# Performance work log

Measured on AMD Instinct MI355X. Metric: run time of the kernel, lower is better.

## Reference

```python
import jax, jax.numpy as jnp
import numpy as np

D_MODEL = 256
N_HEADS = 4
WINDOW = 8
DECAY = 0.9
STEP_SIZE = 0.5


def _linear(x, w, b):
    # torch nn.Linear: y = x @ w.T + b, w: [out, in]
    return jnp.einsum('...i,oi->...o', x, w) + b


def _layernorm(x, scale, bias, eps=1e-5):
    mu = jnp.mean(x, axis=-1, keepdims=True)
    var = jnp.var(x, axis=-1, keepdims=True)
    return (x - mu) * jax.lax.rsqrt(var + eps) * scale + bias


def _ema(x, decay):
    # ema[t] = decay*ema[t-1] + (1-decay)*x[t], ema[-1]=0
    # (exactly the causal conv with weights (1-d)*d^i from the torch code)
    def step(c, xt):
        c = decay * c + (1.0 - decay) * xt
        return c, c
    _, ys = jax.lax.scan(step, jnp.zeros_like(x[:, 0]), jnp.swapaxes(x, 0, 1))
    return jnp.swapaxes(ys, 0, 1)


def setup_inputs() -> dict:
    key = jax.random.key(0)
    ks = iter(jax.random.split(key, 40))
    B, T, D = 8, 1024, D_MODEL
    s = 0.02
    inp = {
        'parallel_repr': jax.random.normal(next(ks), (B, T, D), jnp.float32),
        'sequential_state': jax.random.normal(next(ks), (B, D), jnp.float32),
        'trajectory_summary': jax.random.normal(next(ks), (B, D), jnp.float32),
        # MultiheadAttention params
        'in_proj_w': jax.random.normal(next(ks), (3 * D, D), jnp.float32) * s,
        'in_proj_b': jnp.zeros((3 * D,), jnp.float32),
        'out_proj_w': jax.random.normal(next(ks), (D, D), jnp.float32) * s,
        'out_proj_b': jnp.zeros((D,), jnp.float32),
        # depthwise causal conv (local history)
        'conv_w': jax.random.normal(next(ks), (D, 1, WINDOW), jnp.float32) * s,
        'conv_b': jnp.zeros((D,), jnp.float32),
        # parallel_to_sequential / sequential_to_parallel
        'p2s_w': jax.random.normal(next(ks), (D, D), jnp.float32) * s,
        'p2s_b': jnp.zeros((D,), jnp.float32),
        's2p_w': jax.random.normal(next(ks), (D, D), jnp.float32) * s,
        's2p_b': jnp.zeros((D,), jnp.float32),
        # transition MLP: 3D -> 2D -> D
        'trans_w1': jax.random.normal(next(ks), (2 * D, 3 * D), jnp.float32) * s,
        'trans_b1': jnp.zeros((2 * D,), jnp.float32),
        'trans_w2': jax.random.normal(next(ks), (D, 2 * D), jnp.float32) * s,
        'trans_b2': jnp.zeros((D,), jnp.float32),
        # FFN: D -> 4D -> D
        'ffn_w1': jax.random.normal(next(ks), (4 * D, D), jnp.float32) * s,
        'ffn_b1': jnp.zeros((4 * D,), jnp.float32),
        'ffn_w2': jax.random.normal(next(ks), (D, 4 * D), jnp.float32) * s,
        'ffn_b2': jnp.zeros((D,), jnp.float32),
        # LayerNorms
        'ln1_s': jnp.ones((D,), jnp.float32), 'ln1_b': jnp.zeros((D,), jnp.float32),
        'ln2_s': jnp.ones((D,), jnp.float32), 'ln2_b': jnp.zeros((D,), jnp.float32),
        'ln3_s': jnp.ones((D,), jnp.float32), 'ln3_b': jnp.zeros((D,), jnp.float32),
        'ln4_s': jnp.ones((D,), jnp.float32), 'ln4_b': jnp.zeros((D,), jnp.float32),
    }
    return inp


def _forward(parallel_repr, sequential_state,
             in_proj_w, in_proj_b, out_proj_w, out_proj_b,
             conv_w, conv_b, p2s_w, p2s_b, s2p_w, s2p_b,
             trans_w1, trans_b1, trans_w2, trans_b2,
             ffn_w1, ffn_b1, ffn_w2, ffn_b2,
             ln1_s, ln1_b, ln2_s, ln2_b, ln3_s, ln3_b, ln4_s, ln4_b):
    B, T, D = parallel_repr.shape
    H, hd = N_HEADS, D // N_HEADS

    # --- causal self-attention (nn.MultiheadAttention, batch_first) ---
    qkv = _linear(parallel_repr, in_proj_w, in_proj_b)
    q, k, v = jnp.split(qkv, 3, axis=-1)
    q = q.reshape(B, T, H, hd)
    k = k.reshape(B, T, H, hd)
    v = v.reshape(B, T, H, hd)
    scores = jnp.einsum('bqhd,bkhd->bhqk', q, k) / jnp.sqrt(jnp.asarray(hd, q.dtype))
    causal = jnp.triu(jnp.ones((T, T), bool), 1)
    scores = jnp.where(causal, jnp.finfo(scores.dtype).min, scores)
    attn = jax.nn.softmax(scores, axis=-1)
    attn_out = jnp.einsum('bhqk,bkhd->bqhd', attn, v).reshape(B, T, D)
    attn_out = _linear(attn_out, out_proj_w, out_proj_b)
    x = _layernorm(parallel_repr + attn_out, ln1_s, ln1_b)

    # --- depthwise causal conv (local history) ---
    xt = jnp.swapaxes(x, 1, 2)  # [B, D, T]
    xt_pad = jnp.pad(xt, ((0, 0), (0, 0), (WINDOW - 1, 0)))
    local = jax.lax.conv_general_dilated(
        xt_pad, conv_w, window_strides=(1,), padding='VALID',
        dimension_numbers=('NCH', 'OIH', 'NCH'), feature_group_count=D)
    local_history = jnp.swapaxes(local + conv_b[None, :, None], 1, 2)  # [B, T, D]

    # --- global EMA summary ---
    global_summary = _ema(x, DECAY)

    # --- transition deltas + cumsum state integration ---
    parallel_guidance = _linear(x, p2s_w, p2s_b)
    combined = jnp.concatenate([x + 0.3 * parallel_guidance, local_history, global_summary], axis=-1)
    h = jax.nn.gelu(_linear(combined, trans_w1, trans_b1), approximate=False)
    deltas = _linear(h, trans_w2, trans_b2)
    states = sequential_state[:, None, :] + jnp.cumsum(deltas, axis=1) * STEP_SIZE
    states = _layernorm(states, ln3_s, ln3_b)

    # --- FFN with sequential guidance ---
    seq_guidance = _linear(states, s2p_w, s2p_b)
    f = jax.nn.gelu(_linear(x + 0.3 * seq_guidance, ffn_w1, ffn_b1), approximate=False)
    ffn_out = _linear(f, ffn_w2, ffn_b2)
    x = _layernorm(x + ffn_out, ln2_s, ln2_b)

    final_sequential_state = _layernorm(states[:, -1, :], ln4_s, ln4_b)
    final_trajectory_summary = global_summary[:, -1, :]
    return x, final_sequential_state, final_trajectory_summary


def reference(parallel_repr, sequential_state, trajectory_summary,
              in_proj_w, in_proj_b, out_proj_w, out_proj_b,
              conv_w, conv_b, p2s_w, p2s_b, s2p_w, s2p_b,
              trans_w1, trans_b1, trans_w2, trans_b2,
              ffn_w1, ffn_b1, ffn_w2, ffn_b2,
              ln1_s, ln1_b, ln2_s, ln2_b, ln3_s, ln3_b, ln4_s, ln4_b):
    # trajectory_summary is accepted by the torch forward but never used.
    return _forward(parallel_repr, sequential_state,
                    in_proj_w, in_proj_b, out_proj_w, out_proj_b,
                    conv_w, conv_b, p2s_w, p2s_b, s2p_w, s2p_b,
                    trans_w1, trans_b1, trans_w2, trans_b2,
                    ffn_w1, ffn_b1, ffn_w2, ffn_b2,
                    ln1_s, ln1_b, ln2_s, ln2_b, ln3_s, ln3_b, ln4_s, ln4_b)
```

## Files before the change

kernel.cpp:

```cpp
#include <hip/hip_runtime.h>
#include <math.h>

typedef unsigned short u16;
typedef __attribute__((ext_vector_type(8))) short bf16x8;
typedef __attribute__((ext_vector_type(4))) float f32x4;

#define D_MODEL 256
#define T_SZ 1024
constexpr size_t S_ELT = (size_t)8192 * 256;
constexpr size_t MB = 1024 * 1024;

constexpr size_t OFF_QKV = 0;
constexpr size_t OFF_ATTN = 12 * MB;
constexpr size_t OFF_F = 0;
constexpr size_t OFF_X = 16 * MB;
constexpr size_t OFF_COMB = 24 * MB;
constexpr size_t OFF_FB = 36 * MB;
constexpr size_t OFF_H = 44 * MB;
constexpr size_t OFF_XBF = 48 * MB;
constexpr size_t OFF_WB = 52 * MB;
constexpr size_t OFF_SCR1 = 55 * MB;
constexpr size_t OFF_SCR2 = 55 * MB + 262144;

constexpr int WB_INPROJ = 0;
constexpr int WB_OUTPROJ = 196608;
constexpr int WB_P2S = 262144;
constexpr int WB_S2P = 327680;
constexpr int WB_T1 = 393216;
constexpr int WB_T2 = 786432;
constexpr int WB_F1 = 917504;
constexpr int WB_F2 = 1179648;
constexpr int WB_TOTAL = 1441792;
constexpr int PR_TOTAL = 2097152;

__device__ __forceinline__ u16 f2bf(float f) {
  unsigned int u = __float_as_uint(f);
  u += 0x7fff + ((u >> 16) & 1);
  return (u16)(u >> 16);
}
__device__ __forceinline__ float bf2f(u16 s) {
  return __uint_as_float(((unsigned int)s) << 16);
}

__device__ __forceinline__ void glds16(const u16* g, u16* l) {
  __builtin_amdgcn_global_load_lds(
      (const __attribute__((address_space(1))) void*)g,
      (__attribute__((address_space(3))) void*)l, 16, 0, 0);
}

__global__ __launch_bounds__(256)
void wconv_kernel(const float* w0, const float* w1, const float* w2,
                  const float* w3, const float* w4, const float* w5,
                  const float* w6, const float* w7, const float* pr,
                  u16* __restrict__ wb, u16* __restrict__ prb) {
  const int idx4 = (blockIdx.x * 256 + threadIdx.x) * 4;
  if (idx4 < WB_TOTAL) {
    const int offs[9] = {WB_INPROJ, WB_OUTPROJ, WB_P2S,  WB_S2P, WB_T1,
                         WB_T2,     WB_F1,      WB_F2,   WB_TOTAL};
    const float* srcs[8] = {w0, w1, w2, w3, w4, w5, w6, w7};
    int seg = 0;
    while (idx4 >= offs[seg + 1]) ++seg;
    float4 v = *(const float4*)(srcs[seg] + (idx4 - offs[seg]));
    unsigned int lo = (unsigned int)f2bf(v.x) | ((unsigned int)f2bf(v.y) << 16);
    unsigned int hi = (unsigned int)f2bf(v.z) | ((unsigned int)f2bf(v.w) << 16);
    *(uint2*)(wb + idx4) = make_uint2(lo, hi);
  } else {
    const int i4 = idx4 - WB_TOTAL;
    if (i4 < PR_TOTAL) {
      float4 v = *(const float4*)(pr + i4);
      unsigned int lo = (unsigned int)f2bf(v.x) | ((unsigned int)f2bf(v.y) << 16);
      unsigned int hi = (unsigned int)f2bf(v.z) | ((unsigned int)f2bf(v.w) << 16);
      *(uint2*)(prb + i4) = make_uint2(lo, hi);
    }
  }
}

enum { EPI_NONE = 0, EPI_GELU = 1, EPI_ADDSCALE = 2 };

template <int EPI, int BM, int BN, bool OUTBF, bool VSPLIT>
__global__ __launch_bounds__(256, 4)
void mgemm(const u16* __restrict__ A, int lda,
           const u16* __restrict__ Wb, int K, const float* __restrict__ bias,
           void* __restrict__ Cv, int ldc, int col_off,
           const float* __restrict__ addsrc, u16* __restrict__ vt) {
  __shared__ u16 As[BM * 64];
  __shared__ u16 Bs[BN * 64];
  const int tid = threadIdx.x;
  const int w = tid >> 6, lane = tid & 63;
  const int ln = lane & 15, quad = lane >> 4;
  const int m0 = blockIdx.x * BM;
  const int n0 = blockIdx.y * BN;
  constexpr int MT = (BM == 128) ? 2 : 1;
  const int wm = w * (MT * 16);
  constexpr int wn = 0;
  constexpr int APW = BM / 64;
  constexpr int BPW = BN / 64;

  f32x4 acc[MT][4] = {};

  const int grow = lane >> 2;
  const int gk8 = (lane & 3) * 8;

  for (int k0 = 0; k0 < K; k0 += 64) {
#pragma unroll
    for (int s = 0; s < 2; ++s) {
#pragma unroll
      for (int p = 0; p < APW; ++p) {
        const int g = w * APW + p;
        glds16(A + (size_t)(m0 + g * 16 + grow) * lda + k0 + s * 32 + gk8,
               As + s * BM * 32 + g * 512);
      }
#pragma unroll
      for (int p = 0; p < BPW; ++p) {
        const int g = w * BPW + p;
        glds16(Wb + (size_t)(n0 + g * 16 + grow) * K + k0 + s * 32 + gk8,
               Bs + s * BN * 32 + g * 512);
      }
    }
    __syncthreads();
#pragma unroll
    for (int s = 0; s < 2; ++s) {
      const u16* abase = As + s * BM * 32 + (wm >> 4) * 512 + ln * 32 + quad * 8;
      const u16* bbase = Bs + s * BN * 32 + ln * 32 + quad * 8;
      bf16x8 af[MT], bv[4];
#pragma unroll
      for (int i = 0; i < MT; ++i) af[i] = *(const bf16x8*)(abase + i * 512);
#pragma unroll
      for (int j = 0; j < 4; ++j) bv[j] = *(const bf16x8*)(bbase + j * 512);
#pragma unroll
      for (int i = 0; i < MT; ++i)
#pragma unroll
        for (int j = 0; j < 4; ++j)
          acc[i][j] = __builtin_amdgcn_mfma_f32_16x16x32_bf16(af[i], bv[j],
                                                              acc[i][j], 0, 0, 0);
    }
    __syncthreads();
  }

#pragma unroll
  for (int i = 0; i < MT; ++i)
#pragma unroll
    for (int j = 0; j < 4; ++j) {
      const int col = n0 + wn + j * 16 + ln;
      const float bsv = bias[col];
      const int row0 = m0 + wm + i * 16 + quad * 4;
      float vals[4];
#pragma unroll
      for (int r = 0; r < 4; ++r) {
        float v = acc[i][j][r] + bsv;
        if (EPI == EPI_GELU) v = 0.5f * v * (1.0f + erff(v * 0.70710678f));
        if (EPI == EPI_ADDSCALE)
          v = addsrc[(size_t)(row0 + r) * 256 + col] + 0.3f * v;
        vals[r] = v;
      }
      if (VSPLIT && col >= 512) {
        ushort4 pk;
        pk.x = f2bf(vals[0]); pk.y = f2bf(vals[1]);
        pk.z = f2bf(vals[2]); pk.w = f2bf(vals[3]);
        *(ushort4*)(vt + (size_t)((row0 >> 10) * 256 + (col - 512)) * T_SZ +
                    (row0 & 1023)) = pk;
      } else if (OUTBF) {
#pragma unroll
        for (int r = 0; r < 4; ++r)
          ((u16*)Cv)[(size_t)(row0 + r) * ldc + col_off + col] = f2bf(vals[r]);
      } else {
#pragma unroll
        for (int r = 0; r < 4; ++r)
          ((float*)Cv)[(size_t)(row0 + r) * ldc + col_off + col] = vals[r];
      }
    }
}

__global__ __launch_bounds__(256)
void attn_flash(const u16* __restrict__ qkv, const u16* __restrict__ vt,
                u16* __restrict__ outp) {
  __shared__ u16 Ps[4][16][72];
  const int tid = threadIdx.x;
  const int w = tid >> 6, lane = tid & 63;
  const int ln = lane & 15, quad = lane >> 4, kq8 = quad * 8;
  const int wu = blockIdx.x * 4 + w;
  const int bh = wu >> 6, s = wu & 63;
  const int qt = (s & 1) ? (63 - (s >> 1)) : (s >> 1);
  const int q0 = qt * 16;
  const int b = bh >> 2, h = bh & 3;
  const u16* base = qkv + (size_t)b * T_SZ * 768;
  const u16* vbase = vt + (size_t)bh * 64 * T_SZ;

  bf16x8 qf[2];
#pragma unroll
  for (int ks = 0; ks < 2; ++ks)
    qf[ks] = *(const bf16x8*)(base + (size_t)(q0 + ln) * 768 + h * 64 +
                              ks * 32 + kq8);
  const short ob = (short)0x3F80;
  const bf16x8 ones = {ob, ob, ob, ob, ob, ob, ob, ob};

  f32x4 O[4] = {};
  f32x4 l_acc = {};
  const int ntiles = (qt >> 2) + 1;
  for (int jt = 0; jt < ntiles; ++jt) {
    const int c0 = jt * 64;
    f32x4 sv[4] = {};
#pragma unroll
    for (int ks = 0; ks < 2; ++ks)
#pragma unroll
      for (int j = 0; j < 4; ++j) {
        bf16x8 kf = *(const bf16x8*)(base + (size_t)(c0 + j * 16 + ln) * 768 +
                                     256 + h * 64 + ks * 32 + kq8);
        sv[j] = __builtin_amdgcn_mfma_f32_16x16x32_bf16(qf[ks], kf, sv[j], 0, 0, 0);
      }
    const bool need_mask = (c0 + 63 > q0);
#pragma unroll
    for (int j = 0; j < 4; ++j)
#pragma unroll
      for (int r = 0; r < 4; ++r) {
        float p = __expf(sv[j][r] * 0.125f);
        if (need_mask && (c0 + j * 16 + ln > q0 + quad * 4 + r)) p = 0.f;
        Ps[w][quad * 4 + r][j * 16 + ln] = f2bf(p);
      }
#pragma unroll
    for (int ks = 0; ks < 2; ++ks) {
      bf16x8 pf = *(const bf16x8*)&Ps[w][ln][ks * 32 + kq8];
      l_acc = __builtin_amdgcn_mfma_f32_16x16x32_bf16(pf, ones, l_acc, 0, 0, 0);
#pragma unroll
      for (int j = 0; j < 4; ++j) {
        bf16x8 vf = *(const bf16x8*)(vbase + (size_t)(j * 16 + ln) * T_SZ +
                                     c0 + ks * 32 + kq8);
        O[j] = __builtin_amdgcn_mfma_f32_16x16x32_bf16(pf, vf, O[j], 0, 0, 0);
      }
    }
  }
  u16* op = outp + (size_t)b * T_SZ * 256;
#pragma unroll
  for (int r = 0; r < 4; ++r) {
    const float inv = 1.f / l_acc[r];
#pragma unroll
    for (int j = 0; j < 4; ++j)
      op[(size_t)(q0 + quad * 4 + r) * 256 + h * 64 + j * 16 + ln] =
          f2bf(O[j][r] * inv);
  }
}

__device__ __forceinline__ float block_reduce_sum(float v, float* tmp) {
#pragma unroll
  for (int o = 32; o > 0; o >>= 1) v += __shfl_down(v, o);
  const int lane = threadIdx.x & 63, wid = threadIdx.x >> 6;
  if (lane == 0) tmp[wid] = v;
  __syncthreads();
  v = tmp[0] + tmp[1] + tmp[2] + tmp[3];
  __syncthreads();
  return v;
}

__device__ __forceinline__ float ln_finish(float v, float s1, float s2,
                                           float g, float bb) {
  float mean = s1 * (1.f / 256.f);
  float var = s2 * (1.f / 256.f) - mean * mean;
  return (v - mean) * rsqrtf(var + 1e-5f) * g + bb;
}

__global__ __launch_bounds__(256)
void ln_add_kernel(const float* __restrict__ a, const float* __restrict__ addsrc,
                   const float* __restrict__ g, const float* __restrict__ bb,
                   float* __restrict__ outp, u16* __restrict__ obf) {
  __shared__ float tmp[4];
  const size_t row = blockIdx.x;
  const int d = threadIdx.x;
  float v = a[row * 256 + d] + addsrc[row * 256 + d];
  float s1 = block_reduce_sum(v, tmp);
  float s2 = block_reduce_sum(v * v, tmp);
  float y = ln_finish(v, s1, s2, g[d], bb[d]);
  outp[row * 256 + d] = y;
  if (obf) obf[row * 256 + d] = f2bf(y);
}

__global__ __launch_bounds__(256)
void ln3_states_kernel(const float* __restrict__ deltas, const float* __restrict__ scr,
                       const float* __restrict__ seq, const float* __restrict__ g,
                       const float* __restrict__ bb, u16* __restrict__ st) {
  __shared__ float tmp[4];
  const int row = blockIdx.x;
  const int b = row >> 10, t = row & 1023;
  const int d = threadIdx.x;
  float v = seq[b * 256 + d] +
            0.5f * (deltas[(size_t)row * 256 + d] +
                    scr[(size_t)(b * 32 + (t >> 5)) * 256 + d]);
  float s1 = block_reduce_sum(v, tmp);
  float s2 = block_reduce_sum(v * v, tmp);
  st[(size_t)row * 256 + d] = f2bf(ln_finish(v, s1, s2, g[d], bb[d]));
}

__global__ __launch_bounds__(256)
void ln4_kernel(const u16* __restrict__ st, const float* __restrict__ g,
                const float* __restrict__ bb, float* __restrict__ outp) {
  __shared__ float tmp[4];
  const int b = blockIdx.x, d = threadIdx.x;
  float v = bf2f(st[(size_t)(b * T_SZ + 1023) * 256 + d]);
  float s1 = block_reduce_sum(v, tmp);
  float s2 = block_reduce_sum(v * v, tmp);
  outp[b * 256 + d] = ln_finish(v, s1, s2, g[d], bb[d]);
}

__global__ __launch_bounds__(256)
void emaconv_kernel(const float* __restrict__ x, const float* __restrict__ cw,
                    const float* __restrict__ cb, u16* __restrict__ comb,
                    float* __restrict__ scr) {
  const int bc = blockIdx.x;
  const int b = bc >> 5, ch = bc & 31;
  const int d = threadIdx.x;
  const int t0 = ch * 32;
  float wreg[8];
#pragma unroll
  for (int j = 0; j < 8; ++j) wreg[j] = cw[d * 8 + j];
  const float bias = cb[d];
  float xw[8];
#pragma unroll
  for (int j = 0; j < 7; ++j) {
    const int ts = t0 - 7 + j;
    xw[j] = (ts >= 0) ? x[(size_t)(b * T_SZ + ts) * 256 + d] : 0.f;
  }
  float c = 0.f;
#pragma unroll
  for (int tl = 0; tl < 32; ++tl) {
    const size_t row = (size_t)(b * T_SZ + t0 + tl);
    xw[7] = x[row * 256 + d];
    float conv = bias;
#pragma unroll
    for (int j = 0; j < 8; ++j) conv = fmaf(xw[j], wreg[j], conv);
    c = 0.9f * c + 0.1f * xw[7];
    comb[row * 768 + 256 + d] = f2bf(conv);
    comb[row * 768 + 512 + d] = f2bf(c);
#pragma unroll
    for (int j = 0; j < 7; ++j) xw[j] = xw[j + 1];
  }
  scr[(size_t)bc * 256 + d] = c;
}

__global__ __launch_bounds__(256)
void ema_b_kernel(float* __restrict__ scr) {
  const int b = blockIdx.x, d = threadIdx.x;
  const float q32 = 0.03433683820292512f;
  float carry = 0.f;
  for (int ch = 0; ch < 32; ++ch) {
    const size_t idx = (size_t)(b * 32 + ch) * 256 + d;
    float e = scr[idx];
    scr[idx] = carry;
    carry = e + q32 * carry;
  }
}

__global__ __launch_bounds__(256)
void ema_c_kernel(u16* __restrict__ comb, const float* __restrict__ scr,
                  float* __restrict__ fts) {
  const int row = blockIdx.x;
  const int b = row >> 10, t = row & 1023;
  const int d = threadIdx.x;
  const int ch = t >> 5, tl = t & 31;
  float carry = scr[(size_t)(b * 32 + ch) * 256 + d];
  float l = bf2f(comb[(size_t)row * 768 + 512 + d]);
  float y = fmaf(__powf(0.9f, (float)(tl + 1)), carry, l);
  comb[(size_t)row * 768 + 512 + d] = f2bf(y);
  if (t == 1023) fts[b * 256 + d] = y;
}

__global__ __launch_bounds__(256)
void cs_a_kernel(float* __restrict__ deltas, float* __restrict__ scr) {
  const int bc = blockIdx.x;
  const int b = bc >> 5, ch = bc & 31;
  const int d = threadIdx.x;
  const int t0 = ch * 32;
  float c = 0.f;
  for (int tl = 0; tl < 32; ++tl) {
    const size_t idx = (size_t)(b * T_SZ + t0 + tl) * 256 + d;
    c += deltas[idx];
    deltas[idx] = c;
  }
  scr[(size_t)bc * 256 + d] = c;
}

__global__ __launch_bounds__(256)
void cs_b_kernel(float* __restrict__ scr) {
  const int b = blockIdx.x, d = threadIdx.x;
  float carry = 0.f;
  for (int ch = 0; ch < 32; ++ch) {
    const size_t idx = (size_t)(b * 32 + ch) * 256 + d;
    float e = scr[idx];
    scr[idx] = carry;
    carry += e;
  }
}

extern "C" void kernel_launch(void* const* d_in, const int* in_sizes, int n_in,
                              void* d_out, int out_size, void* d_ws,
                              size_t ws_size, hipStream_t stream) {
  (void)in_sizes; (void)n_in; (void)out_size; (void)ws_size;
  const float* parallel_repr = (const float*)d_in[0];
  const float* sequential_state = (const float*)d_in[1];
  const float* in_proj_b = (const float*)d_in[4];
  const float* out_proj_b = (const float*)d_in[6];
  const float* conv_w = (const float*)d_in[7];
  const float* conv_b = (const float*)d_in[8];
  const float* p2s_b = (const float*)d_in[10];
  const float* s2p_b = (const float*)d_in[12];
  const float* trans_b1 = (const float*)d_in[14];
  const float* trans_b2 = (const float*)d_in[16];
  const float* ffn_b1 = (const float*)d_in[18];
  const float* ffn_b2 = (const float*)d_in[20];
  const float* ln1_s = (const float*)d_in[21];
  const float* ln1_b = (const float*)d_in[22];
  const float* ln2_s = (const float*)d_in[23];
  const float* ln2_b = (const float*)d_in[24];
  const float* ln3_s = (const float*)d_in[25];
  const float* ln3_b = (const float*)d_in[26];
  const float* ln4_s = (const float*)d_in[27];
  const float* ln4_b = (const float*)d_in[28];

  char* ws = (char*)d_ws;
  u16* qkv_bf = (u16*)(ws + OFF_QKV);
  u16* attn_bf = (u16*)(ws + OFF_ATTN);
  u16* states_bf = (u16*)(ws + OFF_ATTN);
  u16* f_bf = (u16*)(ws + OFF_F);
  float* x = (float*)(ws + OFF_X);
  u16* comb = (u16*)(ws + OFF_COMB);
  u16* pr_bf = (u16*)(ws + OFF_COMB);
  u16* ffn_in = (u16*)(ws + OFF_COMB);
  float* fbuf = (float*)(ws + OFF_FB);
  u16* vt = (u16*)(ws + OFF_H);
  u16* h_bf = (u16*)(ws + OFF_H);
  u16* x_bf = (u16*)(ws + OFF_XBF);
  u16* wb = (u16*)(ws + OFF_WB);
  float* scr1 = (float*)(ws + OFF_SCR1);
  float* scr2 = (float*)(ws + OFF_SCR2);
  float* out = (float*)d_out;
  float* out_fss = out + S_ELT;
  float* out_fts = out + S_ELT + 2048;

  const dim3 blk(256);

  wconv_kernel<<<3456, blk, 0, stream>>>(
      (const float*)d_in[3], (const float*)d_in[5], (const float*)d_in[9],
      (const float*)d_in[11], (const float*)d_in[13], (const float*)d_in[15],
      (const float*)d_in[17], (const float*)d_in[19], parallel_repr, wb, pr_bf);
  mgemm<EPI_NONE, 128, 64, true, true><<<dim3(64, 12), blk, 0, stream>>>(
      pr_bf, 256, wb + WB_INPROJ, 256, in_proj_b, qkv_bf, 768, 0, nullptr, vt);
  attn_flash<<<512, blk, 0, stream>>>(qkv_bf, vt, attn_bf);
  mgemm<EPI_NONE, 64, 64, false, false><<<dim3(128, 4), blk, 0, stream>>>(
      attn_bf, 256, wb + WB_OUTPROJ, 256, out_proj_b, fbuf, 256, 0, nullptr,
      nullptr);
  ln_add_kernel<<<8192, blk, 0, stream>>>(parallel_repr, fbuf, ln1_s, ln1_b, x,
                                          x_bf);
  emaconv_kernel<<<256, blk, 0, stream>>>(x, conv_w, conv_b, comb, scr1);
  ema_b_kernel<<<8, blk, 0, stream>>>(scr1);
  ema_c_kernel<<<8192, blk, 0, stream>>>(comb, scr1, out_fts);
  mgemm<EPI_ADDSCALE, 64, 64, true, false><<<dim3(128, 4), blk, 0, stream>>>(
      x_bf, 256, wb + WB_P2S, 256, p2s_b, comb, 768, 0, x, nullptr);
  mgemm<EPI_GELU, 128, 64, true, false><<<dim3(64, 8), blk, 0, stream>>>(
      comb, 768, wb + WB_T1, 768, trans_b1, h_bf, 512, 0, nullptr, nullptr);
  mgemm<EPI_NONE, 64, 64, false, false><<<dim3(128, 4), blk, 0, stream>>>(
      h_bf, 512, wb + WB_T2, 512, trans_b2, fbuf, 256, 0, nullptr, nullptr);
  cs_a_kernel<<<256, blk, 0, stream>>>(fbuf, scr2);
  cs_b_kernel<<<8, blk, 0, stream>>>(scr2);
  ln3_states_kernel<<<8192, blk, 0, stream>>>(fbuf, scr2, sequential_state,
                                              ln3_s, ln3_b, states_bf);
  ln4_kernel<<<8, blk, 0, stream>>>(states_bf, ln4_s, ln4_b, out_fss);
  mgemm<EPI_ADDSCALE, 64, 64, true, false><<<dim3(128, 4), blk, 0, stream>>>(
      states_bf, 256, wb + WB_S2P, 256, s2p_b, ffn_in, 256, 0, x, nullptr);
  mgemm<EPI_GELU, 128, 64, true, false><<<dim3(64, 16), blk, 0, stream>>>(
      ffn_in, 256, wb + WB_F1, 256, ffn_b1, f_bf, 1024, 0, nullptr, nullptr);
  mgemm<EPI_NONE, 64, 64, false, false><<<dim3(128, 4), blk, 0, stream>>>(
      f_bf, 1024, wb + WB_F2, 1024, ffn_b2, fbuf, 256, 0, nullptr, nullptr);
  ln_add_kernel<<<8192, blk, 0, stream>>>(x, fbuf, ln2_s, ln2_b, out, nullptr);
}
```

Before: 275.9 us.

## Fuse LayerNorm into GEMM epilogues and merge scan stages via cooperative launches

Adds a full-row GEMM kernel (64x256 tile) that applies bias, residual add and LayerNorm in its epilogue, replacing the out-proj and FFN2 GEMMs plus their separate ln_add kernels. The three-kernel EMA scan and the cumsum+LN3+LN4 sequence each become a single cooperative kernel that uses grid.sync, keeping per-thread partials in registers instead of round-tripping through global memory. This removes several launches and full-tensor passes, but the fused GEMM runs only 128 blocks (lower occupancy), and the csln kernel performs 32 block reductions serially per block.

```diff
diff --git a/kernel.cpp b/kernel.cpp
--- a/kernel.cpp
+++ b/kernel.cpp
@@ -1,4 +1,5 @@
 #include <hip/hip_runtime.h>
+#include <hip/hip_cooperative_groups.h>
 #include <math.h>
 
 typedef unsigned short u16;
@@ -171,6 +172,92 @@
     }
 }
 
+template <bool WRITE_BF>
+__global__ __launch_bounds__(256, 2)
+void mgemm_ln(const u16* __restrict__ A, const u16* __restrict__ Wb, int K,
+              const float* __restrict__ bias, const float* __restrict__ addsrc,
+              const float* __restrict__ g, const float* __restrict__ bb,
+              float* __restrict__ outf, u16* __restrict__ outbf) {
+  __shared__ u16 As[64 * 64];
+  __shared__ u16 Bs[256 * 64];
+  const int tid = threadIdx.x;
+  const int w = tid >> 6, lane = tid & 63;
+  const int ln = lane & 15, quad = lane >> 4;
+  const int m0 = blockIdx.x * 64;
+  const int grow = lane >> 2;
+  const int gk8 = (lane & 3) * 8;
+
+  f32x4 acc[16] = {};
+
+  for (int k0 = 0; k0 < K; k0 += 64) {
+#pragma unroll
+    for (int s = 0; s < 2; ++s) {
+      glds16(A + (size_t)(m0 + w * 16 + grow) * K + k0 + s * 32 + gk8,
+             As + s * 2048 + w * 512);
+#pragma unroll
+      for (int p = 0; p < 4; ++p) {
+        const int gg = w * 4 + p;
+        glds16(Wb + (size_t)(gg * 16 + grow) * K + k0 + s * 32 + gk8,
+               Bs + s * 8192 + gg * 512);
+      }
+    }
+    __syncthreads();
+#pragma unroll
+    for (int s = 0; s < 2; ++s) {
+      const u16* abase = As + s * 2048 + w * 512 + ln * 32 + quad * 8;
+      const u16* bbase = Bs + s * 8192 + ln * 32 + quad * 8;
+      bf16x8 af = *(const bf16x8*)abase;
+#pragma unroll
+      for (int j = 0; j < 16; ++j) {
+        bf16x8 bv = *(const bf16x8*)(bbase + j * 512);
+        acc[j] = __builtin_amdgcn_mfma_f32_16x16x32_bf16(af, bv, acc[j], 0, 0, 0);
+      }
+    }
+    __syncthreads();
+  }
+
+  const int row0 = m0 + w * 16 + quad * 4;
+  float s1[4] = {}, s2[4] = {};
+#pragma unroll
+  for (int j = 0; j < 16; ++j) {
+    const int col = j * 16 + ln;
+    const float bsv = bias[col];
+#pragma unroll
+    for (int r = 0; r < 4; ++r) {
+      float v = acc[j][r] + bsv + addsrc[(size_t)(row0 + r) * 256 + col];
+      acc[j][r] = v;
+      s1[r] += v;
+      s2[r] += v * v;
+    }
+  }
+#pragma unroll
+  for (int r = 0; r < 4; ++r) {
+#pragma unroll
+    for (int o = 8; o > 0; o >>= 1) {
+      s1[r] += __shfl_xor(s1[r], o);
+      s2[r] += __shfl_xor(s2[r], o);
+    }
+  }
+  float mean[4], inv[4];
+#pragma unroll
+  for (int r = 0; r < 4; ++r) {
+    mean[r] = s1[r] * (1.f / 256.f);
+    float var = s2[r] * (1.f / 256.f) - mean[r] * mean[r];
+    inv[r] = rsqrtf(var + 1e-5f);
+  }
+#pragma unroll
+  for (int j = 0; j < 16; ++j) {
+    const int col = j * 16 + ln;
+    const float gc = g[col], bc = bb[col];
+#pragma unroll
+    for (int r = 0; r < 4; ++r) {
+      const float y = (acc[j][r] - mean[r]) * inv[r] * gc + bc;
+      outf[(size_t)(row0 + r) * 256 + col] = y;
+      if (WRITE_BF) outbf[(size_t)(row0 + r) * 256 + col] = f2bf(y);
+    }
+  }
+}
+
 __global__ __launch_bounds__(256)
 void attn_flash(const u16* __restrict__ qkv, const u16* __restrict__ vt,
                 u16* __restrict__ outp) {
@@ -240,15 +327,18 @@
   }
 }
 
-__device__ __forceinline__ float block_reduce_sum(float v, float* tmp) {
-#pragma unroll
-  for (int o = 32; o > 0; o >>= 1) v += __shfl_down(v, o);
+__device__ __forceinline__ void block_reduce_2(float& a, float& q, float* tmp) {
+#pragma unroll
+  for (int o = 32; o > 0; o >>= 1) {
+    a += __shfl_down(a, o);
+    q += __shfl_down(q, o);
+  }
   const int lane = threadIdx.x & 63, wid = threadIdx.x >> 6;
-  if (lane == 0) tmp[wid] = v;
+  if (lane == 0) { tmp[wid] = a; tmp[4 + wid] = q; }
   __syncthreads();
-  v = tmp[0] + tmp[1] + tmp[2] + tmp[3];
+  a = tmp[0] + tmp[1] + tmp[2] + tmp[3];
+  q = tmp[4] + tmp[5] + tmp[6] + tmp[7];
   __syncthreads();
-  return v;
 }
 
 __device__ __forceinline__ float ln_finish(float v, float s1, float s2,
@@ -259,51 +349,10 @@
 }
 
 __global__ __launch_bounds__(256)
-void ln_add_kernel(const float* __restrict__ a, const float* __restrict__ addsrc,
-                   const float* __restrict__ g, const float* __restrict__ bb,
-                   float* __restrict__ outp, u16* __restrict__ obf) {
-  __shared__ float tmp[4];
-  const size_t row = blockIdx.x;
-  const int d = threadIdx.x;
-  float v = a[row * 256 + d] + addsrc[row * 256 + d];
-  float s1 = block_reduce_sum(v, tmp);
-  float s2 = block_reduce_sum(v * v, tmp);
-  float y = ln_finish(v, s1, s2, g[d], bb[d]);
-  outp[row * 256 + d] = y;
-  if (obf) obf[row * 256 + d] = f2bf(y);
-}
-
-__global__ __launch_bounds__(256)
-void ln3_states_kernel(const float* __restrict__ deltas, const float* __restrict__ scr,
-                       const float* __restrict__ seq, const float* __restrict__ g,
-                       const float* __restrict__ bb, u16* __restrict__ st) {
-  __shared__ float tmp[4];
-  const int row = blockIdx.x;
-  const int b = row >> 10, t = row & 1023;
-  const int d = threadIdx.x;
-  float v = seq[b * 256 + d] +
-            0.5f * (deltas[(size_t)row * 256 + d] +
-                    scr[(size_t)(b * 32 + (t >> 5)) * 256 + d]);
-  float s1 = block_reduce_sum(v, tmp);
-  float s2 = block_reduce_sum(v * v, tmp);
-  st[(size_t)row * 256 + d] = f2bf(ln_finish(v, s1, s2, g[d], bb[d]));
-}
-
-__global__ __launch_bounds__(256)
-void ln4_kernel(const u16* __restrict__ st, const float* __restrict__ g,
-                const float* __restrict__ bb, float* __restrict__ outp) {
-  __shared__ float tmp[4];
-  const int b = blockIdx.x, d = threadIdx.x;
-  float v = bf2f(st[(size_t)(b * T_SZ + 1023) * 256 + d]);
-  float s1 = block_reduce_sum(v, tmp);
-  float s2 = block_reduce_sum(v * v, tmp);
-  outp[b * 256 + d] = ln_finish(v, s1, s2, g[d], bb[d]);
-}
-
-__global__ __launch_bounds__(256)
-void emaconv_kernel(const float* __restrict__ x, const float* __restrict__ cw,
-                    const float* __restrict__ cb, u16* __restrict__ comb,
-                    float* __restrict__ scr) {
+void emaconv_coop(const float* __restrict__ x, const float* __restrict__ cw,
+                  const float* __restrict__ cb, u16* __restrict__ comb,
+                  float* __restrict__ scr, float* __restrict__ fts) {
+  cooperative_groups::grid_group grid = cooperative_groups::this_grid();
   const int bc = blockIdx.x;
   const int b = bc >> 5, ch = bc & 31;
   const int d = threadIdx.x;
@@ -318,6 +367,7 @@
     const int ts = t0 - 7 + j;
     xw[j] = (ts >= 0) ? x[(size_t)(b * T_SZ + ts) * 256 + d] : 0.f;
   }
+  float lreg[32];
   float c = 0.f;
 #pragma unroll
   for (int tl = 0; tl < 32; ++tl) {
@@ -327,65 +377,85 @@
 #pragma unroll
     for (int j = 0; j < 8; ++j) conv = fmaf(xw[j], wreg[j], conv);
     c = 0.9f * c + 0.1f * xw[7];
+    lreg[tl] = c;
     comb[row * 768 + 256 + d] = f2bf(conv);
-    comb[row * 768 + 512 + d] = f2bf(c);
 #pragma unroll
     for (int j = 0; j < 7; ++j) xw[j] = xw[j + 1];
   }
   scr[(size_t)bc * 256 + d] = c;
+  grid.sync();
+  if (bc < 8) {
+    const float q32 = 0.03433683820292512f;
+    float carry = 0.f;
+    for (int chh = 0; chh < 32; ++chh) {
+      const size_t idx = (size_t)(bc * 32 + chh) * 256 + d;
+      float e = scr[idx];
+      scr[idx] = carry;
+      carry = e + q32 * carry;
+    }
+  }
+  grid.sync();
+  const float carry = scr[(size_t)bc * 256 + d];
+  float pw = 0.9f;
+  float ylast = 0.f;
+#pragma unroll
+  for (int tl = 0; tl < 32; ++tl) {
+    const size_t row = (size_t)(b * T_SZ + t0 + tl);
+    const float y = fmaf(pw, carry, lreg[tl]);
+    comb[row * 768 + 512 + d] = f2bf(y);
+    pw *= 0.9f;
+    ylast = y;
+  }
+  if (ch == 31) fts[b * 256 + d] = ylast;
 }
 
 __global__ __launch_bounds__(256)
-void ema_b_kernel(float* __restrict__ scr) {
-  const int b = blockIdx.x, d = threadIdx.x;
-  const float q32 = 0.03433683820292512f;
-  float carry = 0.f;
-  for (int ch = 0; ch < 32; ++ch) {
-    const size_t idx = (size_t)(b * 32 + ch) * 256 + d;
-    float e = scr[idx];
-    scr[idx] = carry;
-    carry = e + q32 * carry;
-  }
-}
-
-__global__ __launch_bounds__(256)
-void ema_c_kernel(u16* __restrict__ comb, const float* __restrict__ scr,
-                  float* __restrict__ fts) {
-  const int row = blockIdx.x;
-  const int b = row >> 10, t = row & 1023;
-  const int d = threadIdx.x;
-  const int ch = t >> 5, tl = t & 31;
-  float carry = scr[(size_t)(b * 32 + ch) * 256 + d];
-  float l = bf2f(comb[(size_t)row * 768 + 512 + d]);
-  float y = fmaf(__powf(0.9f, (float)(tl + 1)), carry, l);
-  comb[(size_t)row * 768 + 512 + d] = f2bf(y);
-  if (t == 1023) fts[b * 256 + d] = y;
-}
-
-__global__ __launch_bounds__(256)
-void cs_a_kernel(float* __restrict__ deltas, float* __restrict__ scr) {
+void csln_coop(const float* __restrict__ deltas, const float* __restrict__ seq,
+               const float* __restrict__ g3, const float* __restrict__ b3,
+               const float* __restrict__ g4, const float* __restrict__ b4,
+               float* __restrict__ scr, u16* __restrict__ st,
+               float* __restrict__ fss) {
+  cooperative_groups::grid_group grid = cooperative_groups::this_grid();
+  __shared__ float tmp[8];
   const int bc = blockIdx.x;
   const int b = bc >> 5, ch = bc & 31;
   const int d = threadIdx.x;
   const int t0 = ch * 32;
+  float cum[32];
   float c = 0.f;
+#pragma unroll
   for (int tl = 0; tl < 32; ++tl) {
-    const size_t idx = (size_t)(b * T_SZ + t0 + tl) * 256 + d;
-    c += deltas[idx];
-    deltas[idx] = c;
+    c += deltas[(size_t)(b * T_SZ + t0 + tl) * 256 + d];
+    cum[tl] = c;
   }
   scr[(size_t)bc * 256 + d] = c;
-}
-
-__global__ __launch_bounds__(256)
-void cs_b_kernel(float* __restrict__ scr) {
-  const int b = blockIdx.x, d = threadIdx.x;
-  float carry = 0.f;
-  for (int ch = 0; ch < 32; ++ch) {
-    const size_t idx = (size_t)(b * 32 + ch) * 256 + d;
-    float e = scr[idx];
-    scr[idx] = carry;
-    carry += e;
+  grid.sync();
+  if (bc < 8) {
+    float carry = 0.f;
+    for (int chh = 0; chh < 32; ++chh) {
+      const size_t idx = (size_t)(bc * 32 + chh) * 256 + d;
+      float e = scr[idx];
+      scr[idx] = carry;
+      carry += e;
+    }
+  }
+  grid.sync();
+  const float carry = scr[(size_t)bc * 256 + d];
+  const float sv = seq[b * 256 + d];
+  const float gg3 = g3[d], bb3 = b3[d];
+#pragma unroll
+  for (int tl = 0; tl < 32; ++tl) {
+    const size_t row = (size_t)(b * T_SZ + t0 + tl);
+    float v = sv + 0.5f * (cum[tl] + carry);
+    float a = v, q = v * v;
+    block_reduce_2(a, q, tmp);
+    const float y = ln_finish(v, a, q, gg3, bb3);
+    st[row * 256 + d] = f2bf(y);
+    if (ch == 31 && tl == 31) {
+      float a2 = y, q2 = y * y;
+      block_reduce_2(a2, q2, tmp);
+      fss[b * 256 + d] = ln_finish(y, a2, q2, g4[d], b4[d]);
+    }
   }
 }
 
@@ -443,30 +513,32 @@
   mgemm<EPI_NONE, 128, 64, true, true><<<dim3(64, 12), blk, 0, stream>>>(
       pr_bf, 256, wb + WB_INPROJ, 256, in_proj_b, qkv_bf, 768, 0, nullptr, vt);
   attn_flash<<<512, blk, 0, stream>>>(qkv_bf, vt, attn_bf);
-  mgemm<EPI_NONE, 64, 64, false, false><<<dim3(128, 4), blk, 0, stream>>>(
-      attn_bf, 256, wb + WB_OUTPROJ, 256, out_proj_b, fbuf, 256, 0, nullptr,
-      nullptr);
-  ln_add_kernel<<<8192, blk, 0, stream>>>(parallel_repr, fbuf, ln1_s, ln1_b, x,
-                                          x_bf);
-  emaconv_kernel<<<256, blk, 0, stream>>>(x, conv_w, conv_b, comb, scr1);
-  ema_b_kernel<<<8, blk, 0, stream>>>(scr1);
-  ema_c_kernel<<<8192, blk, 0, stream>>>(comb, scr1, out_fts);
+  mgemm_ln<true><<<128, blk, 0, stream>>>(
+      attn_bf, wb + WB_OUTPROJ, 256, out_proj_b, parallel_repr, ln1_s, ln1_b,
+      x, x_bf);
+  {
+    void* eargs[] = {(void*)&x, (void*)&conv_w, (void*)&conv_b, (void*)&comb,
+                     (void*)&scr1, (void*)&out_fts};
+    hipLaunchCooperativeKernel(reinterpret_cast<void*>(emaconv_coop),
+                               dim3(256), blk, eargs, 0, stream);
+  }
   mgemm<EPI_ADDSCALE, 64, 64, true, false><<<dim3(128, 4), blk, 0, stream>>>(
       x_bf, 256, wb + WB_P2S, 256, p2s_b, comb, 768, 0, x, nullptr);
   mgemm<EPI_GELU, 128, 64, true, false><<<dim3(64, 8), blk, 0, stream>>>(
       comb, 768, wb + WB_T1, 768, trans_b1, h_bf, 512, 0, nullptr, nullptr);
   mgemm<EPI_NONE, 64, 64, false, false><<<dim3(128, 4), blk, 0, stream>>>(
       h_bf, 512, wb + WB_T2, 512, trans_b2, fbuf, 256, 0, nullptr, nullptr);
-  cs_a_kernel<<<256, blk, 0, stream>>>(fbuf, scr2);
-  cs_b_kernel<<<8, blk, 0, stream>>>(scr2);
-  ln3_states_kernel<<<8192, blk, 0, stream>>>(fbuf, scr2, sequential_state,
-                                              ln3_s, ln3_b, states_bf);
-  ln4_kernel<<<8, blk, 0, stream>>>(states_bf, ln4_s, ln4_b, out_fss);
+  {
+    void* cargs[] = {(void*)&fbuf, (void*)&sequential_state, (void*)&ln3_s,
+                     (void*)&ln3_b, (void*)&ln4_s, (void*)&ln4_b,
+                     (void*)&scr2, (void*)&states_bf, (void*)&out_fss};
+    hipLaunchCooperativeKernel(reinterpret_cast<void*>(csln_coop),
+                               dim3(256), blk, cargs, 0, stream);
+  }
   mgemm<EPI_ADDSCALE, 64, 64, true, false><<<dim3(128, 4), blk, 0, stream>>>(
       states_bf, 256, wb + WB_S2P, 256, s2p_b, ffn_in, 256, 0, x, nullptr);
   mgemm<EPI_GELU, 128, 64, true, false><<<dim3(64, 16), blk, 0, stream>>>(
       ffn_in, 256, wb + WB_F1, 256, ffn_b1, f_bf, 1024, 0, nullptr, nullptr);
-  mgemm<EPI_NONE, 64, 64, false, false><<<dim3(128, 4), blk, 0, stream>>>(
-      f_bf, 1024, wb + WB_F2, 1024, ffn_b2, fbuf, 256, 0, nullptr, nullptr);
-  ln_add_kernel<<<8192, blk, 0, stream>>>(x, fbuf, ln2_s, ln2_b, out, nullptr);
-}
+  mgemm_ln<false><<<128, blk, 0, stream>>>(
+      f_bf, wb + WB_F2, 1024, ffn_b2, x, ln2_s, ln2_b, out, nullptr);
+}
```

Result: slower. 452.4 us (+63.9%).

## Fuse residual-add LayerNorm into output GEMMs and merge LN4 into LN3

Applied to the files above, without the earlier changes.

Adds a GEMM kernel in which each block computes 16 full rows of 256 output columns, so the residual add and LayerNorm run in the epilogue. It replaces the out-proj GEMM plus ln_add and the FFN2 GEMM plus ln_add. It also folds the final LN4 into the LN3 kernel and computes the two reduction sums in one pass. This removes intermediate fp32 round trips through global memory and several launches. In exchange, the 16-row tiles reload the whole weight matrix per block and use 512 blocks, which may lower MFMA efficiency for the K=1024 FFN2 GEMM.

```diff
diff --git a/kernel.cpp b/kernel.cpp
--- a/kernel.cpp
+++ b/kernel.cpp
@@ -171,6 +171,101 @@
     }
 }
 
+template <bool WRITE_BF>
+__global__ __launch_bounds__(256, 4)
+void mgemm_ln16(const u16* __restrict__ A, const u16* __restrict__ Wb, int K,
+                const float* __restrict__ bias, const float* __restrict__ addsrc,
+                const float* __restrict__ g, const float* __restrict__ bb,
+                float* __restrict__ outf, u16* __restrict__ outbf) {
+  __shared__ u16 As[2 * 512];
+  __shared__ u16 Bs[2 * 8192];
+  __shared__ float tS1[4][16], tS2[4][16];
+  const int tid = threadIdx.x;
+  const int w = tid >> 6, lane = tid & 63;
+  const int ln = lane & 15, quad = lane >> 4;
+  const int m0 = blockIdx.x * 16;
+  const int grow = lane >> 2;
+  const int gk8 = (lane & 3) * 8;
+
+  f32x4 acc[4] = {};
+
+  for (int k0 = 0; k0 < K; k0 += 64) {
+    if (w < 2)
+      glds16(A + (size_t)(m0 + grow) * K + k0 + w * 32 + gk8, As + w * 512);
+#pragma unroll
+    for (int p = 0; p < 8; ++p) {
+      const int idx = w * 8 + p;
+      const int s = idx >> 4, gg = idx & 15;
+      glds16(Wb + (size_t)(gg * 16 + grow) * K + k0 + s * 32 + gk8,
+             Bs + s * 8192 + gg * 512);
+    }
+    __syncthreads();
+#pragma unroll
+    for (int s = 0; s < 2; ++s) {
+      const bf16x8 af = *(const bf16x8*)(As + s * 512 + ln * 32 + quad * 8);
+      const u16* bbase = Bs + s * 8192 + (w * 4) * 512 + ln * 32 + quad * 8;
+#pragma unroll
+      for (int j = 0; j < 4; ++j) {
+        bf16x8 bv = *(const bf16x8*)(bbase + j * 512);
+        acc[j] = __builtin_amdgcn_mfma_f32_16x16x32_bf16(af, bv, acc[j], 0, 0, 0);
+      }
+    }
+    __syncthreads();
+  }
+
+  const int row0 = m0 + quad * 4;
+  float s1[4] = {}, s2[4] = {};
+#pragma unroll
+  for (int j = 0; j < 4; ++j) {
+    const int col = w * 64 + j * 16 + ln;
+    const float bsv = bias[col];
+#pragma unroll
+    for (int r = 0; r < 4; ++r) {
+      float v = acc[j][r] + bsv + addsrc[(size_t)(row0 + r) * 256 + col];
+      acc[j][r] = v;
+      s1[r] += v;
+      s2[r] += v * v;
+    }
+  }
+#pragma unroll
+  for (int r = 0; r < 4; ++r) {
+#pragma unroll
+    for (int o = 8; o > 0; o >>= 1) {
+      s1[r] += __shfl_xor(s1[r], o);
+      s2[r] += __shfl_xor(s2[r], o);
+    }
+  }
+  if (ln == 0) {
+#pragma unroll
+    for (int r = 0; r < 4; ++r) {
+      tS1[w][quad * 4 + r] = s1[r];
+      tS2[w][quad * 4 + r] = s2[r];
+    }
+  }
+  __syncthreads();
+  float mean[4], inv[4];
+#pragma unroll
+  for (int r = 0; r < 4; ++r) {
+    const int qr = quad * 4 + r;
+    const float S1 = tS1[0][qr] + tS1[1][qr] + tS1[2][qr] + tS1[3][qr];
+    const float S2 = tS2[0][qr] + tS2[1][qr] + tS2[2][qr] + tS2[3][qr];
+    mean[r] = S1 * (1.f / 256.f);
+    const float var = S2 * (1.f / 256.f) - mean[r] * mean[r];
+    inv[r] = rsqrtf(var + 1e-5f);
+  }
+#pragma unroll
+  for (int j = 0; j < 4; ++j) {
+    const int col = w * 64 + j * 16 + ln;
+    const float gc = g[col], bc = bb[col];
+#pragma unroll
+    for (int r = 0; r < 4; ++r) {
+      const float y = (acc[j][r] - mean[r]) * inv[r] * gc + bc;
+      outf[(size_t)(row0 + r) * 256 + col] = y;
+      if (WRITE_BF) outbf[(size_t)(row0 + r) * 256 + col] = f2bf(y);
+    }
+  }
+}
+
 __global__ __launch_bounds__(256)
 void attn_flash(const u16* __restrict__ qkv, const u16* __restrict__ vt,
                 u16* __restrict__ outp) {
@@ -240,15 +335,18 @@
   }
 }
 
-__device__ __forceinline__ float block_reduce_sum(float v, float* tmp) {
-#pragma unroll
-  for (int o = 32; o > 0; o >>= 1) v += __shfl_down(v, o);
+__device__ __forceinline__ void block_reduce_2(float& a, float& q, float* tmp) {
+#pragma unroll
+  for (int o = 32; o > 0; o >>= 1) {
+    a += __shfl_down(a, o);
+    q += __shfl_down(q, o);
+  }
   const int lane = threadIdx.x & 63, wid = threadIdx.x >> 6;
-  if (lane == 0) tmp[wid] = v;
+  if (lane == 0) { tmp[wid] = a; tmp[4 + wid] = q; }
   __syncthreads();
-  v = tmp[0] + tmp[1] + tmp[2] + tmp[3];
+  a = tmp[0] + tmp[1] + tmp[2] + tmp[3];
+  q = tmp[4] + tmp[5] + tmp[6] + tmp[7];
   __syncthreads();
-  return v;
 }
 
 __device__ __forceinline__ float ln_finish(float v, float s1, float s2,
@@ -256,48 +354,6 @@
   float mean = s1 * (1.f / 256.f);
   float var = s2 * (1.f / 256.f) - mean * mean;
   return (v - mean) * rsqrtf(var + 1e-5f) * g + bb;
-}
-
-__global__ __launch_bounds__(256)
-void ln_add_kernel(const float* __restrict__ a, const float* __restrict__ addsrc,
-                   const float* __restrict__ g, const float* __restrict__ bb,
-                   float* __restrict__ outp, u16* __restrict__ obf) {
-  __shared__ float tmp[4];
-  const size_t row = blockIdx.x;
-  const int d = threadIdx.x;
-  float v = a[row * 256 + d] + addsrc[row * 256 + d];
-  float s1 = block_reduce_sum(v, tmp);
-  float s2 = block_reduce_sum(v * v, tmp);
-  float y = ln_finish(v, s1, s2, g[d], bb[d]);
-  outp[row * 256 + d] = y;
-  if (obf) obf[row * 256 + d] = f2bf(y);
-}
-
-__global__ __launch_bounds__(256)
-void ln3_states_kernel(const float* __restrict__ deltas, const float* __restrict__ scr,
-                       const float* __restrict__ seq, const float* __restrict__ g,
-                       const float* __restrict__ bb, u16* __restrict__ st) {
-  __shared__ float tmp[4];
-  const int row = blockIdx.x;
-  const int b = row >> 10, t = row & 1023;
-  const int d = threadIdx.x;
-  float v = seq[b * 256 + d] +
-            0.5f * (deltas[(size_t)row * 256 + d] +
-                    scr[(size_t)(b * 32 + (t >> 5)) * 256 + d]);
-  float s1 = block_reduce_sum(v, tmp);
-  float s2 = block_reduce_sum(v * v, tmp);
-  st[(size_t)row * 256 + d] = f2bf(ln_finish(v, s1, s2, g[d], bb[d]));
-}
-
-__global__ __launch_bounds__(256)
-void ln4_kernel(const u16* __restrict__ st, const float* __restrict__ g,
-                const float* __restrict__ bb, float* __restrict__ outp) {
-  __shared__ float tmp[4];
-  const int b = blockIdx.x, d = threadIdx.x;
-  float v = bf2f(st[(size_t)(b * T_SZ + 1023) * 256 + d]);
-  float s1 = block_reduce_sum(v, tmp);
-  float s2 = block_reduce_sum(v * v, tmp);
-  outp[b * 256 + d] = ln_finish(v, s1, s2, g[d], bb[d]);
 }
 
 __global__ __launch_bounds__(256)
@@ -386,6 +442,30 @@
     float e = scr[idx];
     scr[idx] = carry;
     carry += e;
+  }
+}
+
+__global__ __launch_bounds__(256)
+void ln3_states_kernel(const float* __restrict__ deltas, const float* __restrict__ scr,
+                       const float* __restrict__ seq, const float* __restrict__ g3,
+                       const float* __restrict__ b3, const float* __restrict__ g4,
+                       const float* __restrict__ b4, u16* __restrict__ st,
+                       float* __restrict__ fss) {
+  __shared__ float tmp[8];
+  const int row = blockIdx.x;
+  const int b = row >> 10, t = row & 1023;
+  const int d = threadIdx.x;
+  float v = seq[b * 256 + d] +
+            0.5f * (deltas[(size_t)row * 256 + d] +
+                    scr[(size_t)(b * 32 + (t >> 5)) * 256 + d]);
+  float a = v, q = v * v;
+  block_reduce_2(a, q, tmp);
+  const float y = ln_finish(v, a, q, g3[d], b3[d]);
+  st[(size_t)row * 256 + d] = f2bf(y);
+  if (t == 1023) {
+    float a2 = y, q2 = y * y;
+    block_reduce_2(a2, q2, tmp);
+    fss[b * 256 + d] = ln_finish(y, a2, q2, g4[d], b4[d]);
   }
 }
 
@@ -443,11 +523,9 @@
   mgemm<EPI_NONE, 128, 64, true, true><<<dim3(64, 12), blk, 0, stream>>>(
       pr_bf, 256, wb + WB_INPROJ, 256, in_proj_b, qkv_bf, 768, 0, nullptr, vt);
   attn_flash<<<512, blk, 0, stream>>>(qkv_bf, vt, attn_bf);
-  mgemm<EPI_NONE, 64, 64, false, false><<<dim3(128, 4), blk, 0, stream>>>(
-      attn_bf, 256, wb + WB_OUTPROJ, 256, out_proj_b, fbuf, 256, 0, nullptr,
-      nullptr);
-  ln_add_kernel<<<8192, blk, 0, stream>>>(parallel_repr, fbuf, ln1_s, ln1_b, x,
-                                          x_bf);
+  mgemm_ln16<true><<<512, blk, 0, stream>>>(
+      attn_bf, wb + WB_OUTPROJ, 256, out_proj_b, parallel_repr, ln1_s, ln1_b,
+      x, x_bf);
   emaconv_kernel<<<256, blk, 0, stream>>>(x, conv_w, conv_b, comb, scr1);
   ema_b_kernel<<<8, blk, 0, stream>>>(scr1);
   ema_c_kernel<<<8192, blk, 0, stream>>>(comb, scr1, out_fts);
@@ -460,13 +538,12 @@
   cs_a_kernel<<<256, blk, 0, stream>>>(fbuf, scr2);
   cs_b_kernel<<<8, blk, 0, stream>>>(scr2);
   ln3_states_kernel<<<8192, blk, 0, stream>>>(fbuf, scr2, sequential_state,
-                                              ln3_s, ln3_b, states_bf);
-  ln4_kernel<<<8, blk, 0, stream>>>(states_bf, ln4_s, ln4_b, out_fss);
+                                              ln3_s, ln3_b, ln4_s, ln4_b,
+                                              states_bf, out_fss);
   mgemm<EPI_ADDSCALE, 64, 64, true, false><<<dim3(128, 4), blk, 0, stream>>>(
       states_bf, 256, wb + WB_S2P, 256, s2p_b, ffn_in, 256, 0, x, nullptr);
   mgemm<EPI_GELU, 128, 64, true, false><<<dim3(64, 16), blk, 0, stream>>>(
       ffn_in, 256, wb + WB_F1, 256, ffn_b1, f_bf, 1024, 0, nullptr, nullptr);
-  mgemm<EPI_NONE, 64, 64, false, false><<<dim3(128, 4), blk, 0, stream>>>(
-      f_bf, 1024, wb + WB_F2, 1024, ffn_b2, fbuf, 256, 0, nullptr, nullptr);
-  ln_add_kernel<<<8192, blk, 0, stream>>>(x, fbuf, ln2_s, ln2_b, out, nullptr);
-}
+  mgemm_ln16<false><<<512, blk, 0, stream>>>(
+      f_bf, wb + WB_F2, 1024, ffn_b2, x, ln2_s, ln2_b, out, nullptr);
+}
```

Result: faster. 260.3 us (-5.7%).
